# Kernel optimization log

Measured on AMD Instinct MI355X. Metric: run time of the kernel, lower is better.

## Reference

```python
import jax, jax.numpy as jnp
import numpy as np

TEMPERATURE = 1.0

def _rope_cos_sin(T, D):
    # inv_freq over even indices 0..D step 2 -> D//2 freqs
    inv_freq = 1.0 / (10000.0 ** (jnp.arange(0, D, 2, dtype=jnp.float32) / D))
    t = jnp.arange(T, dtype=jnp.float32)
    freqs = jnp.einsum('i,j->ij', t, inv_freq)          # [T, D//2]
    emb = jnp.concatenate([freqs, freqs], axis=-1)      # [T, D]
    return jnp.cos(emb), jnp.sin(emb)                   # each [T, D]

def _apply_rope(x, cos, sin):
    # x: [B,H,T,D]; cos/sin: [T,D] broadcast over B,H
    D = x.shape[-1]
    half = D // 2
    x1, x2 = x[..., :half], x[..., half:2 * half]
    c = cos[None, None, :, :half]
    s = sin[None, None, :, :half]
    rot = jnp.concatenate([x1 * c - x2 * s, x1 * s + x2 * c], axis=-1)
    if D > 2 * half:
        rot = jnp.concatenate([rot, x[..., 2 * half:]], axis=-1)
    return rot

def setup_inputs() -> dict:
    key = jax.random.key(0)
    kq, kk, kv = jax.random.split(key, 3)
    B, H, T, D = 2, 16, 2048, 64
    return {
        'q': jax.random.normal(kq, (B, H, T, D), dtype=jnp.float32),
        'k': jax.random.normal(kk, (B, H, T, D), dtype=jnp.float32),
        'v': jax.random.normal(kv, (B, H, T, D), dtype=jnp.float32),
    }

def reference(q, k, v):
    B, H, T, D = q.shape
    cos, sin = _rope_cos_sin(T, D)
    qr = _apply_rope(q, cos, sin)
    kr = _apply_rope(k, cos, sin)
    scale = jnp.sqrt(jnp.float32(D)) * TEMPERATURE
    scores = jnp.einsum('bhtd,bhsd->bhts', qr, kr) / scale  # [B,H,T,T]
    # original subtracts row max then softmax; identical to stable softmax
    attn = jax.nn.softmax(scores, axis=-1)
    out = jnp.einsum('bhts,bhsd->bhtd', attn, v)
    return out, attn
```

## Files before the change

### kernel.cpp

```cpp
#include <hip/hip_runtime.h>
#include <hip/hip_bf16.h>
#include <math.h>


#define T_SEQ  2048
#define D_HEAD 64
#define BH_N   32
#define NCH    32
#define OUT_ELEMS (BH_N * T_SEQ * D_HEAD)

typedef __attribute__((ext_vector_type(8))) short bf16x8;
typedef __attribute__((ext_vector_type(4))) float f32x4;

__device__ __forceinline__ unsigned short f2bf(float x) {
    __hip_bfloat16 h = __float2bfloat16(x);
    return *reinterpret_cast<unsigned short*>(&h);
}

__device__ __forceinline__ int swz(int o) { return o ^ (((o >> 7) & 7) << 4); }

__global__ void rope_table_kernel(float* __restrict__ ctab, float* __restrict__ stab) {
    int i = blockIdx.x * blockDim.x + threadIdx.x;
    if (i >= T_SEQ * 32) return;
    int t = i >> 5;
    int j = i & 31;
    float invf = powf(10000.0f, -(float)j / 32.0f);
    float a = (float)t * invf;
    ctab[i] = cosf(a);
    stab[i] = sinf(a);
}

__global__ __launch_bounds__(256)
void ropebf16_kernel(const float* __restrict__ X, const float* __restrict__ ctab,
                     const float* __restrict__ stab, unsigned short* __restrict__ H,
                     float scale)
{
    const int r  = blockIdx.x * 16 + (threadIdx.x >> 4);
    const int c4 = threadIdx.x & 15;
    const int t  = r & (T_SEQ - 1);
    const float4* xr = (const float4*)(X + (size_t)r * 64);
    float4 a = xr[c4];
    float4 b = xr[c4 ^ 8];
    float4 c = ((const float4*)(ctab + t * 32))[c4 & 7];
    float4 s = ((const float4*)(stab + t * 32))[c4 & 7];
    float4 ro;
    if (c4 < 8) {
        ro.x = a.x * c.x - b.x * s.x; ro.y = a.y * c.y - b.y * s.y;
        ro.z = a.z * c.z - b.z * s.z; ro.w = a.w * c.w - b.w * s.w;
    } else {
        ro.x = a.x * c.x + b.x * s.x; ro.y = a.y * c.y + b.y * s.y;
        ro.z = a.z * c.z + b.z * s.z; ro.w = a.w * c.w + b.w * s.w;
    }
    ushort4 h;
    h.x = f2bf(ro.x * scale); h.y = f2bf(ro.y * scale);
    h.z = f2bf(ro.z * scale); h.w = f2bf(ro.w * scale);
    *(ushort4*)(H + (size_t)r * 64 + c4 * 4) = h;
}

__global__ __launch_bounds__(256)
void vtbf16_kernel(const float* __restrict__ V, unsigned short* __restrict__ Vt)
{
    __shared__ float tile[64][65];
    const int bh = blockIdx.y;
    const int tt = blockIdx.x;
    const float* vg = V + ((size_t)bh * T_SEQ + tt * 64) * 64;
    #pragma unroll
    for (int i = 0; i < 4; ++i) {
        const int row = (threadIdx.x >> 4) + i * 16;
        const int c4  = threadIdx.x & 15;
        float4 a = *(const float4*)(vg + (size_t)row * 64 + c4 * 4);
        tile[row][c4 * 4 + 0] = a.x; tile[row][c4 * 4 + 1] = a.y;
        tile[row][c4 * 4 + 2] = a.z; tile[row][c4 * 4 + 3] = a.w;
    }
    __syncthreads();
    #pragma unroll
    for (int i = 0; i < 4; ++i) {
        const int d   = (threadIdx.x >> 4) + i * 16;
        const int tc4 = threadIdx.x & 15;
        ushort4 h;
        h.x = f2bf(tile[tc4 * 4 + 0][d]);
        h.y = f2bf(tile[tc4 * 4 + 1][d]);
        h.z = f2bf(tile[tc4 * 4 + 2][d]);
        h.w = f2bf(tile[tc4 * 4 + 3][d]);
        *(ushort4*)(Vt + ((size_t)bh * 64 + d) * T_SEQ + tt * 64 + tc4 * 4) = h;
    }
}

__global__ __launch_bounds__(256, 3)
void attn_mfma_kernel(const unsigned short* __restrict__ Qb,
                      const unsigned short* __restrict__ Kb,
                      const unsigned short* __restrict__ Vt,
                      float* __restrict__ out, float* __restrict__ attn)
{
    __shared__ __align__(16) unsigned short kbuf[2][64][64];
    __shared__ __align__(16) unsigned short vbuf[2][64][64];
    __shared__ __align__(16) unsigned short pbuf[4][16][72];

    const int tid  = threadIdx.x;
    const int lane = tid & 63;
    const int w    = tid >> 6;
    const int lrow = lane & 15;
    const int lgrp = lane >> 4;

    const int lid = blockIdx.x;
    const int vid = (lid & 7) * 128 + (lid >> 3);
    const int bh  = vid >> 5;
    const int m   = vid & 31;
    const int t0  = m * 64 + w * 16;

    const size_t base = (size_t)bh * T_SEQ * D_HEAD;
    const char* kgb = (const char*)(Kb + base);
    const char* vgb = (const char*)(Vt + (size_t)bh * 64 * T_SEQ);

    bf16x8 qf0, qf1;
    {
        const unsigned short* qp = Qb + base + (size_t)(t0 + lrow) * 64 + lgrp * 8;
        qf0 = *(const bf16x8*)(qp);
        qf1 = *(const bf16x8*)(qp + 32);
    }

    const int so0 = w * 1024 + lane * 16;
    const int so1 = so0 + 4096;
    const int sq0 = swz(so0);
    const int sq1 = swz(so1);
    char* klds = (char*)&kbuf[0][0][0];
    char* vlds = (char*)&vbuf[0][0][0];
    char* plds = (char*)&pbuf[w][0][0];

#define STAGE_K(b, cc) do { \
    __builtin_amdgcn_global_load_lds((const unsigned int*)(kgb + (size_t)(cc) * 8192 + sq0), \
        (unsigned int*)(klds + (b) * 8192 + w * 1024), 16, 0, 0); \
    __builtin_amdgcn_global_load_lds((const unsigned int*)(kgb + (size_t)(cc) * 8192 + sq1), \
        (unsigned int*)(klds + (b) * 8192 + 4096 + w * 1024), 16, 0, 0); \
} while (0)

#define STAGE_V(b, cc) do { \
    __builtin_amdgcn_global_load_lds((const unsigned int*)(vgb + (size_t)(sq0 >> 7) * 4096 + (cc) * 128 + (sq0 & 127)), \
        (unsigned int*)(vlds + (b) * 8192 + w * 1024), 16, 0, 0); \
    __builtin_amdgcn_global_load_lds((const unsigned int*)(vgb + (size_t)(sq1 >> 7) * 4096 + (cc) * 128 + (sq1 & 127)), \
        (unsigned int*)(vlds + (b) * 8192 + 4096 + w * 1024), 16, 0, 0); \
} while (0)

    float rp = 0.f;
    STAGE_K(0, 0);
    for (int cc = 0; cc < NCH; ++cc) {
        const int p = cc & 1;
        asm volatile("s_waitcnt vmcnt(0)" ::: "memory");
        __builtin_amdgcn_s_barrier();
        if (cc + 1 < NCH) STAGE_K(p ^ 1, cc + 1);
        __builtin_amdgcn_sched_barrier(0);
        const char* kb = klds + p * 8192;
        #pragma unroll
        for (int nt = 0; nt < 4; ++nt) {
            const int o = (nt * 16 + lrow) * 128 + lgrp * 16;
            bf16x8 a0 = *(const bf16x8*)(kb + swz(o));
            bf16x8 a1 = *(const bf16x8*)(kb + swz(o + 64));
            f32x4 acc = (f32x4){0.f, 0.f, 0.f, 0.f};
            acc = __builtin_amdgcn_mfma_f32_16x16x32_bf16(a0, qf0, acc, 0, 0, 0);
            acc = __builtin_amdgcn_mfma_f32_16x16x32_bf16(a1, qf1, acc, 0, 0, 0);
            rp += __expf(acc[0]) + __expf(acc[1]) + __expf(acc[2]) + __expf(acc[3]);
        }
        asm volatile("s_waitcnt lgkmcnt(0)" ::: "memory");
        __builtin_amdgcn_s_barrier();
    }
    rp += __shfl_xor(rp, 16, 64);
    rp += __shfl_xor(rp, 32, 64);
    const float inv = 1.0f / rp;

    f32x4 o4[4];
    #pragma unroll
    for (int nd = 0; nd < 4; ++nd) o4[nd] = (f32x4){0.f, 0.f, 0.f, 0.f};

    float* arow = attn + (size_t)bh * T_SEQ * T_SEQ + (size_t)(t0 + lrow) * T_SEQ + lgrp * 4;

    STAGE_K(0, 0);
    STAGE_V(0, 0);
    asm volatile("s_waitcnt vmcnt(0)" ::: "memory");

    for (int cc = 0; cc < NCH; ++cc) {
        const int p = cc & 1;
        asm volatile("s_waitcnt vmcnt(4)" ::: "memory");
        __builtin_amdgcn_s_barrier();
        if (cc + 1 < NCH) { STAGE_K(p ^ 1, cc + 1); STAGE_V(p ^ 1, cc + 1); }
        __builtin_amdgcn_sched_barrier(0);

        const char* kb = klds + p * 8192;
        const char* vb = vlds + p * 8192;

        f32x4 s4[4];
        #pragma unroll
        for (int nt = 0; nt < 4; ++nt) {
            const int o = (nt * 16 + lrow) * 128 + lgrp * 16;
            bf16x8 a0 = *(const bf16x8*)(kb + swz(o));
            bf16x8 a1 = *(const bf16x8*)(kb + swz(o + 64));
            f32x4 acc = (f32x4){0.f, 0.f, 0.f, 0.f};
            acc = __builtin_amdgcn_mfma_f32_16x16x32_bf16(a0, qf0, acc, 0, 0, 0);
            acc = __builtin_amdgcn_mfma_f32_16x16x32_bf16(a1, qf1, acc, 0, 0, 0);
            s4[nt] = acc;
        }
        #pragma unroll
        for (int nt = 0; nt < 4; ++nt) {
            s4[nt][0] = __expf(s4[nt][0]) * inv;
            s4[nt][1] = __expf(s4[nt][1]) * inv;
            s4[nt][2] = __expf(s4[nt][2]) * inv;
            s4[nt][3] = __expf(s4[nt][3]) * inv;
        }
        #pragma unroll
        for (int nt = 0; nt < 4; ++nt) {
            ushort4 p4;
            p4.x = f2bf(s4[nt][0]); p4.y = f2bf(s4[nt][1]);
            p4.z = f2bf(s4[nt][2]); p4.w = f2bf(s4[nt][3]);
            *(ushort4*)(plds + lrow * 144 + nt * 32 + lgrp * 8) = p4;
        }
        #pragma unroll
        for (int ks = 0; ks < 2; ++ks) {
            bf16x8 pa = *(const bf16x8*)(plds + lrow * 144 + ks * 64 + lgrp * 16);
            #pragma unroll
            for (int nd = 0; nd < 4; ++nd) {
                const int vo = (nd * 16 + lrow) * 128 + ks * 64 + lgrp * 16;
                bf16x8 vf = *(const bf16x8*)(vb + swz(vo));
                o4[nd] = __builtin_amdgcn_mfma_f32_16x16x32_bf16(pa, vf, o4[nd], 0, 0, 0);
            }
        }
        __builtin_amdgcn_sched_barrier(0);
        #pragma unroll
        for (int nt = 0; nt < 4; ++nt)
            __builtin_nontemporal_store(s4[nt], (f32x4*)(arow + cc * 64 + nt * 16));

        asm volatile("s_waitcnt lgkmcnt(0)" ::: "memory");
        __builtin_amdgcn_s_barrier();
    }

    #pragma unroll
    for (int nd = 0; nd < 4; ++nd)
        #pragma unroll
        for (int j = 0; j < 4; ++j)
            __builtin_nontemporal_store(o4[nd][j],
                out + base + (size_t)(t0 + lgrp * 4 + j) * D_HEAD + nd * 16 + lrow);

#undef STAGE_K
#undef STAGE_V
}

extern "C" void kernel_launch(void* const* d_in, const int* in_sizes, int n_in,
                              void* d_out, int out_size, void* d_ws, size_t ws_size,
                              hipStream_t stream) {
    const float* q = (const float*)d_in[0];
    const float* k = (const float*)d_in[1];
    const float* v = (const float*)d_in[2];
    float* out  = (float*)d_out;
    float* attn = out + (size_t)OUT_ELEMS;

    float* ctab = (float*)d_ws;
    float* stab = ctab + T_SEQ * 32;
    unsigned short* wsu = (unsigned short*)(stab + T_SEQ * 32);
    const size_t NE = (size_t)BH_N * T_SEQ * D_HEAD;
    unsigned short* Qb = wsu + 0 * NE;
    unsigned short* Kb = wsu + 1 * NE;
    unsigned short* Vt = wsu + 2 * NE;

    rope_table_kernel<<<dim3((T_SEQ * 32 + 255) / 256), dim3(256), 0, stream>>>(ctab, stab);
    ropebf16_kernel<<<dim3(BH_N * T_SEQ / 16), dim3(256), 0, stream>>>(q, ctab, stab, Qb, 0.125f);
    ropebf16_kernel<<<dim3(BH_N * T_SEQ / 16), dim3(256), 0, stream>>>(k, ctab, stab, Kb, 1.0f);
    vtbf16_kernel<<<dim3(T_SEQ / 64, BH_N), dim3(256), 0, stream>>>(v, Vt);
    attn_mfma_kernel<<<dim3(BH_N * T_SEQ / 64), dim3(256), 0, stream>>>(Qb, Kb, Vt, out, attn);
}
```

Baseline: 215.0 us.

## Triple-buffer K in LDS, load V fragments directly to registers, drop trailing barriers

Result: faster. 210.0 us (-2.3%).

```diff
diff --git a/kernel.cpp b/kernel.cpp
--- a/kernel.cpp
+++ b/kernel.cpp
@@ -86,14 +86,13 @@
     }
 }
 
-__global__ __launch_bounds__(256, 3)
+__global__ __launch_bounds__(256, 4)
 void attn_mfma_kernel(const unsigned short* __restrict__ Qb,
                       const unsigned short* __restrict__ Kb,
                       const unsigned short* __restrict__ Vt,
                       float* __restrict__ out, float* __restrict__ attn)
 {
-    __shared__ __align__(16) unsigned short kbuf[2][64][64];
-    __shared__ __align__(16) unsigned short vbuf[2][64][64];
+    __shared__ __align__(16) unsigned short kbuf[3][64][64];
     __shared__ __align__(16) unsigned short pbuf[4][16][72];
 
     const int tid  = threadIdx.x;
@@ -110,7 +109,7 @@
 
     const size_t base = (size_t)bh * T_SEQ * D_HEAD;
     const char* kgb = (const char*)(Kb + base);
-    const char* vgb = (const char*)(Vt + (size_t)bh * 64 * T_SEQ);
+    const unsigned short* vgb = Vt + (size_t)bh * 64 * T_SEQ;
 
     bf16x8 qf0, qf1;
     {
@@ -124,7 +123,6 @@
     const int sq0 = swz(so0);
     const int sq1 = swz(so1);
     char* klds = (char*)&kbuf[0][0][0];
-    char* vlds = (char*)&vbuf[0][0][0];
     char* plds = (char*)&pbuf[w][0][0];
 
 #define STAGE_K(b, cc) do { \
@@ -134,22 +132,16 @@
         (unsigned int*)(klds + (b) * 8192 + 4096 + w * 1024), 16, 0, 0); \
 } while (0)
 
-#define STAGE_V(b, cc) do { \
-    __builtin_amdgcn_global_load_lds((const unsigned int*)(vgb + (size_t)(sq0 >> 7) * 4096 + (cc) * 128 + (sq0 & 127)), \
-        (unsigned int*)(vlds + (b) * 8192 + w * 1024), 16, 0, 0); \
-    __builtin_amdgcn_global_load_lds((const unsigned int*)(vgb + (size_t)(sq1 >> 7) * 4096 + (cc) * 128 + (sq1 & 127)), \
-        (unsigned int*)(vlds + (b) * 8192 + 4096 + w * 1024), 16, 0, 0); \
-} while (0)
-
-    float rp = 0.f;
+    float rpa0 = 0.f, rpa1 = 0.f, rpa2 = 0.f, rpa3 = 0.f;
     STAGE_K(0, 0);
+    STAGE_K(1, 1);
     for (int cc = 0; cc < NCH; ++cc) {
-        const int p = cc & 1;
-        asm volatile("s_waitcnt vmcnt(0)" ::: "memory");
+        if (cc < NCH - 1) { asm volatile("s_waitcnt vmcnt(2)" ::: "memory"); }
+        else              { asm volatile("s_waitcnt vmcnt(0)" ::: "memory"); }
         __builtin_amdgcn_s_barrier();
-        if (cc + 1 < NCH) STAGE_K(p ^ 1, cc + 1);
-        __builtin_amdgcn_sched_barrier(0);
-        const char* kb = klds + p * 8192;
+        if (cc + 2 < NCH) STAGE_K((cc + 2) % 3, cc + 2);
+        __builtin_amdgcn_sched_barrier(0);
+        const char* kb = klds + (cc % 3) * 8192;
         #pragma unroll
         for (int nt = 0; nt < 4; ++nt) {
             const int o = (nt * 16 + lrow) * 128 + lgrp * 16;
@@ -158,15 +150,18 @@
             f32x4 acc = (f32x4){0.f, 0.f, 0.f, 0.f};
             acc = __builtin_amdgcn_mfma_f32_16x16x32_bf16(a0, qf0, acc, 0, 0, 0);
             acc = __builtin_amdgcn_mfma_f32_16x16x32_bf16(a1, qf1, acc, 0, 0, 0);
-            rp += __expf(acc[0]) + __expf(acc[1]) + __expf(acc[2]) + __expf(acc[3]);
-        }
-        asm volatile("s_waitcnt lgkmcnt(0)" ::: "memory");
-        __builtin_amdgcn_s_barrier();
-    }
+            rpa0 += __expf(acc[0]); rpa1 += __expf(acc[1]);
+            rpa2 += __expf(acc[2]); rpa3 += __expf(acc[3]);
+        }
+    }
+    float rp = (rpa0 + rpa1) + (rpa2 + rpa3);
     rp += __shfl_xor(rp, 16, 64);
     rp += __shfl_xor(rp, 32, 64);
     const float inv = 1.0f / rp;
 
+    __builtin_amdgcn_sched_barrier(0);
+    __builtin_amdgcn_s_barrier();
+
     f32x4 o4[4];
     #pragma unroll
     for (int nd = 0; nd < 4; ++nd) o4[nd] = (f32x4){0.f, 0.f, 0.f, 0.f};
@@ -174,19 +169,23 @@
     float* arow = attn + (size_t)bh * T_SEQ * T_SEQ + (size_t)(t0 + lrow) * T_SEQ + lgrp * 4;
 
     STAGE_K(0, 0);
-    STAGE_V(0, 0);
-    asm volatile("s_waitcnt vmcnt(0)" ::: "memory");
+    STAGE_K(1, 1);
+    asm volatile("s_waitcnt vmcnt(2)" ::: "memory");
 
     for (int cc = 0; cc < NCH; ++cc) {
-        const int p = cc & 1;
-        asm volatile("s_waitcnt vmcnt(4)" ::: "memory");
         __builtin_amdgcn_s_barrier();
-        if (cc + 1 < NCH) { STAGE_K(p ^ 1, cc + 1); STAGE_V(p ^ 1, cc + 1); }
-        __builtin_amdgcn_sched_barrier(0);
-
-        const char* kb = klds + p * 8192;
-        const char* vb = vlds + p * 8192;
-
+        __builtin_amdgcn_sched_barrier(0);
+        bf16x8 vf[8];
+        #pragma unroll
+        for (int nd = 0; nd < 4; ++nd)
+            #pragma unroll
+            for (int ks = 0; ks < 2; ++ks)
+                vf[nd * 2 + ks] = *(const bf16x8*)(vgb + (size_t)(nd * 16 + lrow) * T_SEQ
+                                                   + cc * 64 + ks * 32 + lgrp * 8);
+        if (cc + 2 < NCH) STAGE_K((cc + 2) % 3, cc + 2);
+        __builtin_amdgcn_sched_barrier(0);
+
+        const char* kb = klds + (cc % 3) * 8192;
         f32x4 s4[4];
         #pragma unroll
         for (int nt = 0; nt < 4; ++nt) {
@@ -212,23 +211,18 @@
             p4.z = f2bf(s4[nt][2]); p4.w = f2bf(s4[nt][3]);
             *(ushort4*)(plds + lrow * 144 + nt * 32 + lgrp * 8) = p4;
         }
+        asm volatile("s_waitcnt lgkmcnt(0)" ::: "memory");
+        __builtin_amdgcn_sched_barrier(0);
+        #pragma unroll
+        for (int nt = 0; nt < 4; ++nt)
+            __builtin_nontemporal_store(s4[nt], (f32x4*)(arow + cc * 64 + nt * 16));
         #pragma unroll
         for (int ks = 0; ks < 2; ++ks) {
             bf16x8 pa = *(const bf16x8*)(plds + lrow * 144 + ks * 64 + lgrp * 16);
             #pragma unroll
-            for (int nd = 0; nd < 4; ++nd) {
-                const int vo = (nd * 16 + lrow) * 128 + ks * 64 + lgrp * 16;
-                bf16x8 vf = *(const bf16x8*)(vb + swz(vo));
-                o4[nd] = __builtin_amdgcn_mfma_f32_16x16x32_bf16(pa, vf, o4[nd], 0, 0, 0);
-            }
-        }
-        __builtin_amdgcn_sched_barrier(0);
-        #pragma unroll
-        for (int nt = 0; nt < 4; ++nt)
-            __builtin_nontemporal_store(s4[nt], (f32x4*)(arow + cc * 64 + nt * 16));
-
-        asm volatile("s_waitcnt lgkmcnt(0)" ::: "memory");
-        __builtin_amdgcn_s_barrier();
+            for (int nd = 0; nd < 4; ++nd)
+                o4[nd] = __builtin_amdgcn_mfma_f32_16x16x32_bf16(pa, vf[nd * 2 + ks], o4[nd], 0, 0, 0);
+        }
     }
 
     #pragma unroll
@@ -239,7 +233,6 @@
                 out + base + (size_t)(t0 + lgrp * 4 + j) * D_HEAD + nd * 16 + lrow);
 
 #undef STAGE_K
-#undef STAGE_V
 }
 
 extern "C" void kernel_launch(void* const* d_in, const int* in_sizes, int n_in,
```
